# Performance work log

Hardware: AMD Instinct MI355X
Metric: run time of the kernel (lower is better)

## Reference

```python
import jax, jax.numpy as jnp
import numpy as np
from jax import lax

VOCAB, E, H = 50257, 512, 512
B, S = 32, 512


def setup_inputs() -> dict:
    key = jax.random.key(0)
    ks = jax.random.split(key, 9)
    inv_e = 1.0 / np.sqrt(E + H)
    return {
        "sequence": jax.random.randint(ks[0], (B, S), 0, VOCAB),
        "enc_out": jax.random.normal(ks[1], (B, S, H), dtype=jnp.float32),
        "enc_h": jax.random.normal(ks[2], (1, B, H), dtype=jnp.float32),
        "enc_c": jax.random.normal(ks[3], (1, B, H), dtype=jnp.float32),
        "emb_table": jax.random.normal(ks[4], (VOCAB, E), dtype=jnp.float32),
        "W_ih": jax.random.uniform(ks[5], (4 * H, E + H), minval=-inv_e, maxval=inv_e, dtype=jnp.float32),
        "W_hh": jax.random.uniform(ks[6], (4 * H, H), minval=-inv_e, maxval=inv_e, dtype=jnp.float32),
        "b_ih": jax.random.uniform(ks[7], (4 * H,), minval=-inv_e, maxval=inv_e, dtype=jnp.float32),
        "b_hh": jax.random.uniform(ks[8], (4 * H,), minval=-inv_e, maxval=inv_e, dtype=jnp.float32),
    }


def reference(sequence, enc_out, enc_h, enc_c, emb_table, W_ih, W_hh, b_ih, b_hh):
    # NOTE: faithful to source: the (h, c) state fed to the LSTMCell every
    # timestep is always (enc_h[0], enc_c[0]); only the previous hidden is
    # recycled by concatenation into the cell input.
    b, s = sequence.shape
    e = emb_table.shape[1]
    h = W_hh.shape[1]
    embedded = emb_table[sequence]                      # [B,S,E]
    h0 = enc_h[0]                                       # [B,H] (constant cell-state h)
    c0 = enc_c[0]                                       # [B,H] (constant cell-state c)
    # Precompute constant contribution from (h0, biases) and the big batched
    # GEMM for the embedding half of the input once, outside the scan.
    const = h0 @ W_hh.T + b_hh + b_ih                   # [B,4H]
    W_e = W_ih[:, :e]                                   # [4H,E]
    W_h = W_ih[:, e:]                                   # [4H,H]
    emb_gates = jnp.einsum('bse,ge->sbg', embedded, W_e)  # [S,B,4H]

    def step(prev_h, emb_g_t):
        gates = emb_g_t + prev_h @ W_h.T + const        # [B,4H]
        i, f, g, o = jnp.split(gates, 4, axis=-1)       # torch gate order i,f,g,o
        i = jax.nn.sigmoid(i)
        f = jax.nn.sigmoid(f)
        g = jnp.tanh(g)
        o = jax.nn.sigmoid(o)
        c_new = f * c0 + i * g
        h_new = o * jnp.tanh(c_new)
        return h_new, h_new

    _, hs = lax.scan(step, jnp.zeros_like(h0), emb_gates)   # hs: [S,B,H]
    out = jnp.transpose(hs, (1, 0, 2)).reshape(b, s * h)    # torch.cat(outs, dim=1)
    return out
```

## Files before the change

kernel.cpp:

```cpp
#include <hip/hip_runtime.h>
#include <stdint.h>

#define EDIM  512
#define HDIM  512
#define BSZ   32
#define SLEN  512
#define GDIM  2048
#define TEAMS 2
#define TWG   32

#define SENT 0xFFFFFFFFFFFFFFFFull

typedef __bf16 bf16x8 __attribute__((ext_vector_type(8)));
typedef float  f32x4  __attribute__((ext_vector_type(4)));

__device__ __forceinline__ uint16_t f2bf(float f) {
  union { float f; uint32_t i; } v; v.f = f;
  uint32_t r = v.i + 0x7FFFu + ((v.i >> 16) & 1u);
  return (uint16_t)(r >> 16);
}
__device__ __forceinline__ float bf2f(uint32_t u) {
  union { uint32_t i; float f; } v; v.i = u << 16; return v.f;
}
union BF8 { uint16_t u[8]; uint4 v; bf16x8 b; unsigned long long q[2]; };
union BF4 { uint16_t u[4]; unsigned long long q; };
__device__ __forceinline__ uint4 pack8(float4 lo, float4 hi) {
  BF8 r;
  r.u[0] = f2bf(lo.x); r.u[1] = f2bf(lo.y); r.u[2] = f2bf(lo.z); r.u[3] = f2bf(lo.w);
  r.u[4] = f2bf(hi.x); r.u[5] = f2bf(hi.y); r.u[6] = f2bf(hi.z); r.u[7] = f2bf(hi.w);
  return r.v;
}
__device__ __forceinline__ float sigm(float x) { return 1.0f / (1.0f + __expf(-x)); }
__device__ __forceinline__ float tanh_(float x) {
  float ax = fabsf(x);
  float e  = __expf(2.0f * ax);
  float t  = 1.0f - 2.0f / (e + 1.0f);
  return copysignf(t, x);
}
__device__ __forceinline__ unsigned long long allc64(const unsigned long long* p) {
  return __hip_atomic_load(p, __ATOMIC_RELAXED, __HIP_MEMORY_SCOPE_AGENT);
}

__global__ __launch_bounds__(256) void k_const(
    const float* __restrict__ Whh, const float* __restrict__ h0,
    const float* __restrict__ bih, const float* __restrict__ bhh,
    float* __restrict__ cgb)
{
  int idx = blockIdx.x * 256 + threadIdx.x;
  int g = idx >> 5, b = idx & 31;
  const float4* w4 = (const float4*)(Whh + (size_t)g * HDIM);
  const float4* h4 = (const float4*)(h0  + (size_t)b * HDIM);
  float acc = 0.f;
  #pragma unroll 8
  for (int k = 0; k < HDIM / 4; k++) {
    float4 a = w4[k], c = h4[k];
    acc += a.x * c.x + a.y * c.y + a.z * c.z + a.w * c.w;
  }
  acc += bih[g] + bhh[g];
  cgb[idx] = acc;
}

__global__ __launch_bounds__(256) void k_emb(
    const int* __restrict__ seq, const float* __restrict__ emb,
    const float* __restrict__ Wih, const float* __restrict__ cgb,
    uint16_t* __restrict__ eg)
{
  __shared__ uint4 wlds[4096];
  const int tid = threadIdx.x;
  const int gc  = blockIdx.x & 31;
  const int sc  = blockIdx.x >> 5;
  const int g0  = gc * 64, s0 = sc * 4;

  for (int i = tid; i < 64 * 64; i += 256) {
    int n = i >> 6, c = i & 63;
    const float* wp = Wih + (size_t)(g0 + n) * 1024 + c * 8;
    float4 lo = *(const float4*)(wp);
    float4 hi = *(const float4*)(wp + 4);
    wlds[(((n >> 4) * 16 + (c >> 2)) << 6) + ((n & 15) << 2) + (c & 3)] = pack8(lo, hi);
  }
  __syncthreads();

  const int lane = tid & 63, w = tid >> 6;
  const int q = lane >> 4, nl = lane & 15;
  const int Nt  = w & 1;
  const int Mt0 = (w >> 1) * 2;
  const int bcol = Nt * 16 + nl;

  float c0i[4], c1i[4];
  #pragma unroll
  for (int r = 0; r < 4; r++) {
    c0i[r] = cgb[(g0 + (Mt0    ) * 16 + q * 4 + r) * 32 + bcol];
    c1i[r] = cgb[(g0 + (Mt0 + 1) * 16 + q * 4 + r) * 32 + bcol];
  }

  for (int si = 0; si < 4; si++) {
    int s = s0 + si;
    int rowi = seq[bcol * SLEN + s];
    const float* brow = emb + (size_t)rowi * EDIM + q * 8;
    f32x4 acc0, acc1;
    #pragma unroll
    for (int r = 0; r < 4; r++) { acc0[r] = c0i[r]; acc1[r] = c1i[r]; }
    #pragma unroll 4
    for (int kc = 0; kc < 16; kc++) {
      float4 blo = *(const float4*)(brow + kc * 32);
      float4 bhi = *(const float4*)(brow + kc * 32 + 4);
      BF8 bf; bf.v = pack8(blo, bhi);
      BF8 a0; a0.v = wlds[(((Mt0    ) * 16 + kc) << 6) + (nl << 2) + q];
      BF8 a1; a1.v = wlds[(((Mt0 + 1) * 16 + kc) << 6) + (nl << 2) + q];
      acc0 = __builtin_amdgcn_mfma_f32_16x16x32_bf16(a0.b, bf.b, acc0, 0, 0, 0);
      acc1 = __builtin_amdgcn_mfma_f32_16x16x32_bf16(a1.b, bf.b, acc1, 0, 0, 0);
    }
    #pragma unroll
    for (int r = 0; r < 4; r++) {
      int m0 = (Mt0    ) * 16 + q * 4 + r;
      int m1 = (Mt0 + 1) * 16 + q * 4 + r;
      eg[((size_t)s * 32 + bcol) * GDIM + g0 + m0] = f2bf(acc0[r]);
      eg[((size_t)s * 32 + bcol) * GDIM + g0 + m1] = f2bf(acc1[r]);
    }
  }
}

__global__ __launch_bounds__(64) void k_scan(
    const float* __restrict__ Wih, const float* __restrict__ c0,
    const uint16_t* __restrict__ eg, unsigned long long* __restrict__ hist,
    float* __restrict__ out)
{
  const int bid  = blockIdx.x;
  const int team = bid & 7;
  if (team >= TEAMS) return;
  const int wg   = bid >> 3;

  __shared__ uint4 wlds[4096];
  const int tid = threadIdx.x;
  const int j0  = wg * 16;

  for (int i = tid; i < 64 * 64; i += 64) {
    int n = i >> 6, c = i & 63;
    int grow = (n >> 4) * HDIM + j0 + (n & 15);
    const float* wp = Wih + (size_t)grow * 1024 + 512 + c * 8;
    float4 lo = *(const float4*)(wp);
    float4 hi = *(const float4*)(wp + 4);
    wlds[(((n >> 4) * 16 + (c >> 2)) << 6) + ((n & 15) << 2) + (c & 3)] = pack8(lo, hi);
  }

  const int lane = tid;
  const int q = lane >> 4, nl = lane & 15;
  const int b  = team * 16 + nl;
  const int jq = j0 + q * 4;
  const int jblk = wg * 4 + q;
  unsigned long long* ht = hist + (size_t)team * SLEN * 2048;
  float c0r[4];
  #pragma unroll
  for (int r = 0; r < 4; r++) c0r[r] = c0[(size_t)b * HDIM + jq + r];
  __syncthreads();

  ushort4 egv[4], egp[4];
  #pragma unroll
  for (int nt = 0; nt < 4; nt++)
    egv[nt] = *(const ushort4*)(eg + ((size_t)0 * 32 + b) * GDIM + nt * HDIM + jq);

  for (int t = 0; t < SLEN; t++) {
    const int tn = (t + 1 < SLEN) ? t + 1 : t;
    #pragma unroll
    for (int nt = 0; nt < 4; nt++)
      egp[nt] = *(const ushort4*)(eg + ((size_t)tn * 32 + b) * GDIM + nt * HDIM + jq);

    f32x4 acc[4];
    #pragma unroll
    for (int nt = 0; nt < 4; nt++) {
      acc[nt][0] = bf2f(egv[nt].x); acc[nt][1] = bf2f(egv[nt].y);
      acc[nt][2] = bf2f(egv[nt].z); acc[nt][3] = bf2f(egv[nt].w);
    }

    if (t > 0) {
      const unsigned long long* hp = ht + (size_t)(t - 1) * 2048 + nl;
      unsigned long long v[32];
      #pragma unroll
      for (int kc = 0; kc < 16; kc++) {
        v[2 * kc]     = hp[(kc * 8 + q * 2    ) * 16];
        v[2 * kc + 1] = hp[(kc * 8 + q * 2 + 1) * 16];
      }
      bool any = false;
      #pragma unroll
      for (int i = 0; i < 32; i++) any |= (v[i] == SENT);
      while (__any(any)) {
        #pragma unroll
        for (int kc = 0; kc < 16; kc++) {
          v[2 * kc]     = allc64(hp + (kc * 8 + q * 2    ) * 16);
          v[2 * kc + 1] = allc64(hp + (kc * 8 + q * 2 + 1) * 16);
        }
        any = false;
        #pragma unroll
        for (int i = 0; i < 32; i++) any |= (v[i] == SENT);
      }

      #pragma unroll
      for (int kc = 0; kc < 16; kc++) {
        BF8 hf; hf.q[0] = v[2 * kc]; hf.q[1] = v[2 * kc + 1];
        #pragma unroll
        for (int nt = 0; nt < 4; nt++) {
          BF8 af; af.v = wlds[((nt * 16 + kc) << 6) + (nl << 2) + q];
          acc[nt] = __builtin_amdgcn_mfma_f32_16x16x32_bf16(af.b, hf.b, acc[nt], 0, 0, 0);
        }
      }
    }

    float4 ov;
    BF4 hb;
    {
      float i0 = sigm(acc[0][0]), f0 = sigm(acc[1][0]), g0v = tanh_(acc[2][0]), o0 = sigm(acc[3][0]);
      float i1 = sigm(acc[0][1]), f1 = sigm(acc[1][1]), g1v = tanh_(acc[2][1]), o1 = sigm(acc[3][1]);
      float i2 = sigm(acc[0][2]), f2 = sigm(acc[1][2]), g2v = tanh_(acc[2][2]), o2 = sigm(acc[3][2]);
      float i3 = sigm(acc[0][3]), f3 = sigm(acc[1][3]), g3v = tanh_(acc[2][3]), o3 = sigm(acc[3][3]);
      ov.x = o0 * tanh_(f0 * c0r[0] + i0 * g0v);
      ov.y = o1 * tanh_(f1 * c0r[1] + i1 * g1v);
      ov.z = o2 * tanh_(f2 * c0r[2] + i2 * g2v);
      ov.w = o3 * tanh_(f3 * c0r[3] + i3 * g3v);
      hb.u[0] = f2bf(ov.x); hb.u[1] = f2bf(ov.y); hb.u[2] = f2bf(ov.z); hb.u[3] = f2bf(ov.w);
    }
    unsigned long long* dst = ht + (size_t)t * 2048 + (size_t)jblk * 16 + nl;
    *dst = hb.q;
    __hip_atomic_store(dst, hb.q, __ATOMIC_RELAXED, __HIP_MEMORY_SCOPE_AGENT);
    *(float4*)(out + (size_t)b * (SLEN * HDIM) + (size_t)t * HDIM + jq) = ov;

    #pragma unroll
    for (int nt = 0; nt < 4; nt++) egv[nt] = egp[nt];
  }
}

extern "C" void kernel_launch(void* const* d_in, const int* in_sizes, int n_in,
                              void* d_out, int out_size, void* d_ws, size_t ws_size,
                              hipStream_t stream)
{
  (void)in_sizes; (void)n_in; (void)out_size; (void)ws_size;
  const int*   seq  = (const int*)d_in[0];
  const float* ench = (const float*)d_in[2];
  const float* encc = (const float*)d_in[3];
  const float* emb  = (const float*)d_in[4];
  const float* Wih  = (const float*)d_in[5];
  const float* Whh  = (const float*)d_in[6];
  const float* bih  = (const float*)d_in[7];
  const float* bhh  = (const float*)d_in[8];
  float* out = (float*)d_out;

  char* ws = (char*)d_ws;
  float*    cgb   = (float*)ws;
  uint16_t* eg    = (uint16_t*)(ws + 264192);
  unsigned long long* hist = (unsigned long long*)(ws + 67373056);

  hipMemsetAsync(hist, 0xFF, (size_t)TEAMS * SLEN * 2048 * 8, stream);
  k_const<<<dim3(256),  dim3(256), 0, stream>>>(Whh, ench, bih, bhh, cgb);
  k_emb  <<<dim3(4096), dim3(256), 0, stream>>>(seq, emb, Wih, cgb, eg);
  k_scan <<<dim3(256),  dim3(64),  0, stream>>>(Wih, encc, eg, hist, out);
}
```

Before: 1.962 ms.

## Keep recurrent weights in registers and alternate cache-bypassing polls in scan

Each scan workgroup now holds its W_h slice as 64 bf16x8 fragments in VGPRs instead of LDS. This removes the LDS reads ahead of every MFMA on the serial critical path, and launch_bounds(64,1) gives the compiler the register budget for it. The spin-wait poll now alternates between inline-asm global loads with the sc0 bit and the existing atomic loads, with an explicit waitcnt, to change how the hidden-state hand-off between workgroups is observed. The eg prefetch for the next timestep is dropped, so its load latency now falls inside each step, and the polling change depends on hand-written cache bits and a waitcnt encoding.

Result: no change. 1.991 ms (+1.5%).

```diff
diff --git a/kernel.cpp b/kernel.cpp
--- a/kernel.cpp
+++ b/kernel.cpp
@@ -39,6 +39,10 @@
 }
 __device__ __forceinline__ unsigned long long allc64(const unsigned long long* p) {
   return __hip_atomic_load(p, __ATOMIC_RELAXED, __HIP_MEMORY_SCOPE_AGENT);
+}
+__device__ __forceinline__ void l2c64_issue(const unsigned long long* p,
+                                            unsigned long long& r) {
+  asm volatile("global_load_dwordx2 %0, %1, off sc0" : "=v"(r) : "v"(p));
 }
 
 __global__ __launch_bounds__(256) void k_const(
@@ -120,7 +124,7 @@
   }
 }
 
-__global__ __launch_bounds__(64) void k_scan(
+__global__ __launch_bounds__(64, 1) void k_scan(
     const float* __restrict__ Wih, const float* __restrict__ c0,
     const uint16_t* __restrict__ eg, unsigned long long* __restrict__ hist,
     float* __restrict__ out)
@@ -129,41 +133,35 @@
   const int team = bid & 7;
   if (team >= TEAMS) return;
   const int wg   = bid >> 3;
-
-  __shared__ uint4 wlds[4096];
-  const int tid = threadIdx.x;
-  const int j0  = wg * 16;
-
-  for (int i = tid; i < 64 * 64; i += 64) {
-    int n = i >> 6, c = i & 63;
-    int grow = (n >> 4) * HDIM + j0 + (n & 15);
-    const float* wp = Wih + (size_t)grow * 1024 + 512 + c * 8;
-    float4 lo = *(const float4*)(wp);
-    float4 hi = *(const float4*)(wp + 4);
-    wlds[(((n >> 4) * 16 + (c >> 2)) << 6) + ((n & 15) << 2) + (c & 3)] = pack8(lo, hi);
-  }
-
-  const int lane = tid;
+  const int j0   = wg * 16;
+
+  const int lane = threadIdx.x;
   const int q = lane >> 4, nl = lane & 15;
   const int b  = team * 16 + nl;
   const int jq = j0 + q * 4;
   const int jblk = wg * 4 + q;
   unsigned long long* ht = hist + (size_t)team * SLEN * 2048;
+
+  BF8 af[4][16];
+  #pragma unroll
+  for (int nt = 0; nt < 4; nt++) {
+    const float* rowp = Wih + (size_t)(nt * HDIM + j0 + nl) * 1024 + 512 + q * 8;
+    #pragma unroll
+    for (int kc = 0; kc < 16; kc++) {
+      float4 lo = *(const float4*)(rowp + kc * 32);
+      float4 hi = *(const float4*)(rowp + kc * 32 + 4);
+      af[nt][kc].v = pack8(lo, hi);
+    }
+  }
   float c0r[4];
   #pragma unroll
   for (int r = 0; r < 4; r++) c0r[r] = c0[(size_t)b * HDIM + jq + r];
-  __syncthreads();
-
-  ushort4 egv[4], egp[4];
-  #pragma unroll
-  for (int nt = 0; nt < 4; nt++)
-    egv[nt] = *(const ushort4*)(eg + ((size_t)0 * 32 + b) * GDIM + nt * HDIM + jq);
 
   for (int t = 0; t < SLEN; t++) {
-    const int tn = (t + 1 < SLEN) ? t + 1 : t;
+    ushort4 egv[4];
     #pragma unroll
     for (int nt = 0; nt < 4; nt++)
-      egp[nt] = *(const ushort4*)(eg + ((size_t)tn * 32 + b) * GDIM + nt * HDIM + jq);
+      egv[nt] = *(const ushort4*)(eg + ((size_t)t * 32 + b) * GDIM + nt * HDIM + jq);
 
     f32x4 acc[4];
     #pragma unroll
@@ -183,12 +181,24 @@
       bool any = false;
       #pragma unroll
       for (int i = 0; i < 32; i++) any |= (v[i] == SENT);
+      int pass = 0;
       while (__any(any)) {
-        #pragma unroll
-        for (int kc = 0; kc < 16; kc++) {
-          v[2 * kc]     = allc64(hp + (kc * 8 + q * 2    ) * 16);
-          v[2 * kc + 1] = allc64(hp + (kc * 8 + q * 2 + 1) * 16);
+        if ((pass & 1) == 0) {
+          #pragma unroll
+          for (int kc = 0; kc < 16; kc++) {
+            l2c64_issue(hp + (kc * 8 + q * 2    ) * 16, v[2 * kc]);
+            l2c64_issue(hp + (kc * 8 + q * 2 + 1) * 16, v[2 * kc + 1]);
+          }
+          __builtin_amdgcn_s_waitcnt(0x0F70);
+          __builtin_amdgcn_sched_barrier(0);
+        } else {
+          #pragma unroll
+          for (int kc = 0; kc < 16; kc++) {
+            v[2 * kc]     = allc64(hp + (kc * 8 + q * 2    ) * 16);
+            v[2 * kc + 1] = allc64(hp + (kc * 8 + q * 2 + 1) * 16);
+          }
         }
+        pass++;
         any = false;
         #pragma unroll
         for (int i = 0; i < 32; i++) any |= (v[i] == SENT);
@@ -198,10 +208,8 @@
       for (int kc = 0; kc < 16; kc++) {
         BF8 hf; hf.q[0] = v[2 * kc]; hf.q[1] = v[2 * kc + 1];
         #pragma unroll
-        for (int nt = 0; nt < 4; nt++) {
-          BF8 af; af.v = wlds[((nt * 16 + kc) << 6) + (nl << 2) + q];
-          acc[nt] = __builtin_amdgcn_mfma_f32_16x16x32_bf16(af.b, hf.b, acc[nt], 0, 0, 0);
-        }
+        for (int nt = 0; nt < 4; nt++)
+          acc[nt] = __builtin_amdgcn_mfma_f32_16x16x32_bf16(af[nt][kc].b, hf.b, acc[nt], 0, 0, 0);
       }
     }
 
@@ -222,9 +230,6 @@
     *dst = hb.q;
     __hip_atomic_store(dst, hb.q, __ATOMIC_RELAXED, __HIP_MEMORY_SCOPE_AGENT);
     *(float4*)(out + (size_t)b * (SLEN * HDIM) + (size_t)t * HDIM + jq) = ov;
-
-    #pragma unroll
-    for (int nt = 0; nt < 4; nt++) egv[nt] = egp[nt];
   }
 }
 
```
